# Performance work log

Measured on AMD Instinct MI355X. Metric: run time of the kernel, lower is better.

The kernel has to match this reference:

```python
import jax, jax.numpy as jnp
import numpy as np

N = 1_000_000          # points
C_IN = 10              # decorated point features
C_OUT = 64             # pillar feature channels
S = 30_000             # number of pillars (segments)
EPS = 1e-3             # BatchNorm1d eps


def setup_inputs() -> dict:
    key = jax.random.key(0)
    ks = jax.random.split(key, 8)
    inputs = jax.random.normal(ks[0], (N, C_IN), dtype=jnp.float32)
    # every pillar gets ~N/S points; sorted, all segments non-empty
    unq_inv = jnp.sort(jnp.arange(N, dtype=jnp.int32) % S)
    W_lin = jax.random.normal(ks[1], (C_OUT, C_IN), dtype=jnp.float32) * 0.3
    gamma = 1.0 + 0.1 * jax.random.normal(ks[2], (C_OUT,), dtype=jnp.float32)
    beta = 0.1 * jax.random.normal(ks[3], (C_OUT,), dtype=jnp.float32)
    dw1 = jax.random.normal(ks[4], (C_OUT,), dtype=jnp.float32) * 0.5      # depthwise 1x1 conv (groups=C)
    pw1 = jax.random.normal(ks[5], (C_OUT, C_OUT), dtype=jnp.float32) * 0.1  # pointwise 1x1 conv
    dw2 = jax.random.normal(ks[6], (C_OUT,), dtype=jnp.float32) * 0.5
    pw2 = jax.random.normal(ks[7], (C_OUT, C_OUT), dtype=jnp.float32) * 0.1
    return {"inputs": inputs, "unq_inv": unq_inv, "W_lin": W_lin,
            "gamma": gamma, "beta": beta, "dw1": dw1, "pw1": pw1,
            "dw2": dw2, "pw2": pw2}


def reference(inputs, unq_inv, W_lin, gamma, beta, dw1, pw1, dw2, pw2):
    # Linear (no bias) -> BN (training-mode batch stats) -> ReLU
    x = inputs @ W_lin.T                                   # [N, C]
    mu = jnp.mean(x, axis=0)
    var = jnp.mean(jnp.square(x - mu), axis=0)             # biased var, as torch BN
    x = (x - mu) * jax.lax.rsqrt(var + EPS) * gamma + beta
    x = jax.nn.relu(x)

    # MAFF attention: local branch (depthwise scale -> swish -> 1x1 conv)
    s = x * dw1                                            # groups=C 1x1 conv == per-channel scale
    xl = (s * jax.nn.sigmoid(s)) @ pw1.T                   # [N, C]
    # global branch: avg-pool over points -> depthwise scale -> relu -> 1x1 conv
    g = jnp.mean(x, axis=0)                                # [C]
    xg = pw2 @ jax.nn.relu(dw2 * g)                        # [C]
    wei = jax.nn.sigmoid(xl + xg)                          # broadcast [N,C] + [C]
    xi = x * (1.0 + wei)

    # segment reductions keyed by pillar id (scatter_max + scatter_sum)
    x_max = jax.ops.segment_max(xi, unq_inv, num_segments=S,
                                indices_are_sorted=True)
    x_sum = jax.ops.segment_sum(xi, unq_inv, num_segments=S,
                                indices_are_sorted=True)
    return x_max + x_sum                                   # [S, C]
```

## Files before the change

kernel.cpp:

```cpp
#include <hip/hip_runtime.h>
#include <math.h>

#define N_PTS   1000000
#define CI      10
#define C       64
#define NSEG    30000
#define BN_EPS  1e-3f


using f32x4 = __attribute__((ext_vector_type(4))) float;
using s16x8 = __attribute__((ext_vector_type(8))) short;

__device__ inline short f2bf(float x) {
    unsigned u = __float_as_uint(x);
    unsigned r = (u + 0x7fffu + ((u >> 16) & 1u)) >> 16;
    return (short)r;
}
__device__ inline unsigned pack_trunc(float lo, float hi) {
    return (__float_as_uint(hi) & 0xffff0000u) | (__float_as_uint(lo) >> 16);
}
__device__ inline float frcp(float x) { return __builtin_amdgcn_rcpf(x); }

__global__ void __launch_bounds__(256) k_moments(const float* __restrict__ inp,
                                                 const int* __restrict__ idx,
                                                 float* __restrict__ ws,
                                                 int* __restrict__ starts) {
    const int tid = threadIdx.x;
    float v[65];
#pragma unroll
    for (int k = 0; k < 65; ++k) v[k] = 0.f;

    for (int p = blockIdx.x * blockDim.x + tid; p < N_PTS; p += gridDim.x * blockDim.x) {
        const float2* r2 = (const float2*)(inp + (size_t)p * CI);
        float2 a0 = r2[0], a1 = r2[1], a2 = r2[2], a3 = r2[3], a4 = r2[4];
        float r[CI] = {a0.x, a0.y, a1.x, a1.y, a2.x, a2.y, a3.x, a3.y, a4.x, a4.y};
#pragma unroll
        for (int i = 0; i < CI; ++i) v[i] += r[i];
        int kk = 10;
#pragma unroll
        for (int i = 0; i < CI; ++i)
#pragma unroll
            for (int j = i; j < CI; ++j) { v[kk] = fmaf(r[i], r[j], v[kk]); ++kk; }

        int iv = idx[p];
        if (p == 0) starts[0] = 0;
        else if (idx[p - 1] != iv) starts[iv] = p;
    }

#pragma unroll
    for (int k = 0; k < 65; ++k) {
#pragma unroll
        for (int off = 32; off >= 1; off >>= 1)
            v[k] += __shfl_xor(v[k], off, 64);
    }
    __shared__ float red[4 * 65];
    const int wv = tid >> 6, ln = tid & 63;
    if (ln == 0) {
#pragma unroll
        for (int k = 0; k < 65; ++k) red[wv * 65 + k] = v[k];
    }
    __syncthreads();
    if (tid < 65)
        atomicAdd(&ws[tid], red[tid] + red[65 + tid] + red[130 + tid] + red[195 + tid]);
}

__global__ void k_finalize(const float* __restrict__ W,
                           const float* __restrict__ gamma,
                           const float* __restrict__ beta,
                           float* __restrict__ ws) {
    const int c = threadIdx.x;
    float w[CI];
#pragma unroll
    for (int i = 0; i < CI; ++i) w[i] = W[c * CI + i];
    const float inv_n = 1.f / (float)N_PTS;

    float mu = 0.f;
#pragma unroll
    for (int i = 0; i < CI; ++i) mu = fmaf(w[i], ws[i], mu);
    mu *= inv_n;

    float ex2 = 0.f;
    int kk = 10;
#pragma unroll
    for (int i = 0; i < CI; ++i)
#pragma unroll
        for (int j = i; j < CI; ++j) {
            float m = ws[kk];
            float t = w[i] * w[j] * m;
            ex2 += (i == j) ? t : 2.f * t;
            ++kk;
        }
    ex2 *= inv_n;

    float var = ex2 - mu * mu;
    float rstd = rsqrtf(var + BN_EPS);
    float a = rstd * gamma[c];
    ws[128 + c] = a;
    ws[192 + c] = beta[c] - mu * a;
#pragma unroll
    for (int i = 0; i < CI; ++i) ws[384 + c * CI + i] = a * w[i];
}

__global__ void __launch_bounds__(256) k_gstats(const float* __restrict__ inp,
                                                float* __restrict__ ws) {
    const int tid  = threadIdx.x;
    const int oct  = tid & 7;
    const int slot = (tid & 63) >> 3;

    float w[8][CI], bv[8];
#pragma unroll
    for (int j = 0; j < 8; ++j) {
        const int c = oct * 8 + j;
#pragma unroll
        for (int i = 0; i < CI; ++i) w[j][i] = ws[384 + c * CI + i];
        bv[j] = ws[192 + c];
    }

    float acc[8];
#pragma unroll
    for (int j = 0; j < 8; ++j) acc[j] = 0.f;

    const int wid = (blockIdx.x * blockDim.x + tid) >> 6;
    const int nw  = (gridDim.x * blockDim.x) >> 6;
    for (int pb = wid * 8; pb < N_PTS; pb += nw * 8) {
        const int p = pb + slot;
        const float2* r2 = (const float2*)(inp + (size_t)p * CI);
        float2 a0 = r2[0], a1 = r2[1], a2 = r2[2], a3 = r2[3], a4 = r2[4];
        float r[CI] = {a0.x, a0.y, a1.x, a1.y, a2.x, a2.y, a3.x, a3.y, a4.x, a4.y};
#pragma unroll
        for (int j = 0; j < 8; ++j) {
            float x = bv[j];
#pragma unroll
            for (int i = 0; i < CI; ++i) x = fmaf(w[j][i], r[i], x);
            acc[j] += fmaxf(x, 0.f);
        }
    }

#pragma unroll
    for (int j = 0; j < 8; ++j) {
        acc[j] += __shfl_xor(acc[j], 8, 64);
        acc[j] += __shfl_xor(acc[j], 16, 64);
        acc[j] += __shfl_xor(acc[j], 32, 64);
    }
    __shared__ float red[4 * 64];
    const int wv = tid >> 6, ln = tid & 63;
    if (ln < 8) {
#pragma unroll
        for (int j = 0; j < 8; ++j) red[wv * 64 + ln * 8 + j] = acc[j];
    }
    __syncthreads();
    if (tid < 64)
        atomicAdd(&ws[256 + tid], red[tid] + red[64 + tid] + red[128 + tid] + red[192 + tid]);
}

__global__ void k_xg(const float* __restrict__ dw2,
                     const float* __restrict__ pw2,
                     float* __restrict__ ws) {
    __shared__ float t[C];
    const int c = threadIdx.x;
    float g = ws[256 + c] * (1.f / (float)N_PTS);
    t[c] = fmaxf(dw2[c] * g, 0.f);
    __syncthreads();
    float acc = 0.f;
#pragma unroll
    for (int k = 0; k < C; ++k) acc = fmaf(pw2[c * C + k], t[k], acc);
    ws[320 + c] = acc;
}

#define LD 68
__global__ void __launch_bounds__(128) k_main(const float* __restrict__ inp,
                                              const float* __restrict__ dw1,
                                              const float* __restrict__ pw1,
                                              const float* __restrict__ ws,
                                              const int* __restrict__ starts,
                                              float* __restrict__ out) {
    const int tid  = threadIdx.x;
    const int wv   = tid >> 6;
    const int lane = tid & 63;
    const int m = lane & 15;
    const int q = lane >> 4;

    s16x8 wfr[4];
#pragma unroll
    for (int nt = 0; nt < 4; ++nt) {
        s16x8 t;
#pragma unroll
        for (int j = 0; j < 8; ++j) {
            int k = 8 * q + j;
            t[j] = (k < CI) ? f2bf(ws[384 + (nt * 16 + m) * CI + k]) : (short)0;
        }
        wfr[nt] = t;
    }

    s16x8 bfr[4][2];
#pragma unroll
    for (int nt = 0; nt < 4; ++nt)
#pragma unroll
        for (int kc = 0; kc < 2; ++kc) {
            const float* src = pw1 + (nt * 16 + m) * C + kc * 32 + q * 8;
            float4 p0 = *(const float4*)src;
            float4 p1 = *(const float4*)(src + 4);
            s16x8 t;
            t[0] = f2bf(p0.x); t[1] = f2bf(p0.y); t[2] = f2bf(p0.z); t[3] = f2bf(p0.w);
            t[4] = f2bf(p1.x); t[5] = f2bf(p1.y); t[6] = f2bf(p1.z); t[7] = f2bf(p1.w);
            bfr[nt][kc] = t;
        }

    float bb[4], d1v[4], xgv[4];
#pragma unroll
    for (int nt = 0; nt < 4; ++nt) {
        bb[nt]  = ws[192 + nt * 16 + m];
        d1v[nt] = dw1[nt * 16 + m];
        xgv[nt] = ws[320 + nt * 16 + m];
    }

    __shared__ float sb[2][16 * LD];
    float* my = sb[wv];
    const f32x4 zero = {0.f, 0.f, 0.f, 0.f};

    const int gw = blockIdx.x * 2 + wv;
    for (int s = gw; s < NSEG; s += 15000) {
        const int start = starts[s];
        const int end   = (s + 1 < NSEG) ? starts[s + 1] : N_PTS;

        float sm[4]  = {0.f, 0.f, 0.f, 0.f};
        float mxv[4] = {-INFINITY, -INFINITY, -INFINITY, -INFINITY};

        for (int base = start; base < end; base += 16) {
            const int nb = min(16, end - base);

            const int p = min(base + m, N_PTS - 1);
            const float* row = inp + (size_t)p * CI;
            s16x8 afr = {0, 0, 0, 0, 0, 0, 0, 0};
            if (q == 0) {
                float2 r0 = *(const float2*)(row + 0);
                float2 r1 = *(const float2*)(row + 2);
                float2 r2 = *(const float2*)(row + 4);
                float2 r3 = *(const float2*)(row + 6);
                afr[0] = f2bf(r0.x); afr[1] = f2bf(r0.y);
                afr[2] = f2bf(r1.x); afr[3] = f2bf(r1.y);
                afr[4] = f2bf(r2.x); afr[5] = f2bf(r2.y);
                afr[6] = f2bf(r3.x); afr[7] = f2bf(r3.y);
            } else if (q == 1) {
                float2 r4 = *(const float2*)(row + 8);
                afr[0] = f2bf(r4.x); afr[1] = f2bf(r4.y);
            }

            f32x4 xt[4];
#pragma unroll
            for (int nt = 0; nt < 4; ++nt)
                xt[nt] = __builtin_amdgcn_mfma_f32_16x16x32_bf16(afr, wfr[nt], zero, 0, 0, 0);

            float xn[4][4];
#pragma unroll
            for (int nt = 0; nt < 4; ++nt)
#pragma unroll
                for (int r = 0; r < 4; ++r) {
                    float x = fmaxf(xt[nt][r] + bb[nt], 0.f);
                    xn[nt][r] = x;
                    float sg = x * d1v[nt];
                    float sw = sg * frcp(1.f + __expf(-sg));
                    my[(4 * q + r) * LD + nt * 16 + m] = sw;
                }
            __threadfence_block();

            s16x8 av[2];
#pragma unroll
            for (int kc = 0; kc < 2; ++kc) {
                const float* src = &my[m * LD + kc * 32 + q * 8];
                float4 p0 = *(const float4*)src;
                float4 p1 = *(const float4*)(src + 4);
                union { s16x8 v; unsigned u[4]; } t;
                t.u[0] = pack_trunc(p0.x, p0.y);
                t.u[1] = pack_trunc(p0.z, p0.w);
                t.u[2] = pack_trunc(p1.x, p1.y);
                t.u[3] = pack_trunc(p1.z, p1.w);
                av[kc] = t.v;
            }

            f32x4 xl[4];
#pragma unroll
            for (int nt = 0; nt < 4; ++nt) {
                xl[nt] = __builtin_amdgcn_mfma_f32_16x16x32_bf16(av[0], bfr[nt][0], zero, 0, 0, 0);
                xl[nt] = __builtin_amdgcn_mfma_f32_16x16x32_bf16(av[1], bfr[nt][1], xl[nt], 0, 0, 0);
            }
            __threadfence_block();

#pragma unroll
            for (int nt = 0; nt < 4; ++nt)
#pragma unroll
                for (int r = 0; r < 4; ++r) {
                    float v   = xl[nt][r] + xgv[nt];
                    float wei = frcp(1.f + __expf(-v));
                    float x   = xn[nt][r];
                    float xi  = fmaf(x, wei, x);
                    bool act  = (4 * q + r) < nb;
                    sm[nt]  += act ? xi : 0.f;
                    mxv[nt]  = fmaxf(mxv[nt], act ? xi : -INFINITY);
                }
        }

#pragma unroll
        for (int nt = 0; nt < 4; ++nt) {
            sm[nt] += __shfl_xor(sm[nt], 16, 64);
            sm[nt] += __shfl_xor(sm[nt], 32, 64);
            mxv[nt] = fmaxf(mxv[nt], __shfl_xor(mxv[nt], 16, 64));
            mxv[nt] = fmaxf(mxv[nt], __shfl_xor(mxv[nt], 32, 64));
        }
        float S = sm[0], M = mxv[0];
        if (q == 1) { S = sm[1]; M = mxv[1]; }
        if (q == 2) { S = sm[2]; M = mxv[2]; }
        if (q == 3) { S = sm[3]; M = mxv[3]; }
        out[(size_t)s * C + lane] = S + M;
    }
}

extern "C" void kernel_launch(void* const* d_in, const int* in_sizes, int n_in,
                              void* d_out, int out_size, void* d_ws, size_t ws_size,
                              hipStream_t stream) {
    const float* inp   = (const float*)d_in[0];
    const int*   unq   = (const int*)d_in[1];
    const float* W     = (const float*)d_in[2];
    const float* gamma = (const float*)d_in[3];
    const float* beta  = (const float*)d_in[4];
    const float* dw1   = (const float*)d_in[5];
    const float* pw1   = (const float*)d_in[6];
    const float* dw2   = (const float*)d_in[7];
    const float* pw2   = (const float*)d_in[8];
    float* out = (float*)d_out;
    float* ws  = (float*)d_ws;
    int* starts = (int*)ws + 1024;

    hipMemsetAsync(ws, 0, 384 * sizeof(float), stream);

    k_moments <<<512, 256, 0, stream>>>(inp, unq, ws, starts);
    k_finalize<<<1,   64,  0, stream>>>(W, gamma, beta, ws);
    k_gstats  <<<256, 256, 0, stream>>>(inp, ws);
    k_xg      <<<1,   64,  0, stream>>>(dw2, pw2, ws);
    k_main    <<<7500, 128, 0, stream>>>(inp, dw1, pw1, ws, starts, out);
}
```

Before: 310.2 us.

## Pack multiple pillars per wave and use MFMA for global-stat pass

k_main now gives each wave six consecutive segments and walks their points as one contiguous stream of 16-row tiles, splitting a tile across a segment boundary with masks and flushing per segment. This fills MFMA tiles that per-segment processing left partly empty and adds software prefetch of the next tile's rows. k_gstats is rewritten to compute the linear layer with bf16 MFMA and a prefetched row load, replacing the scalar FMA loop, and grid sizes are adjusted. The cost is more complex boundary logic and extra bf16 rounding in the global mean.

```diff
diff --git a/kernel.cpp b/kernel.cpp
--- a/kernel.cpp
+++ b/kernel.cpp
@@ -104,50 +104,81 @@
 __global__ void __launch_bounds__(256) k_gstats(const float* __restrict__ inp,
                                                 float* __restrict__ ws) {
     const int tid  = threadIdx.x;
-    const int oct  = tid & 7;
-    const int slot = (tid & 63) >> 3;
-
-    float w[8][CI], bv[8];
-#pragma unroll
-    for (int j = 0; j < 8; ++j) {
-        const int c = oct * 8 + j;
-#pragma unroll
-        for (int i = 0; i < CI; ++i) w[j][i] = ws[384 + c * CI + i];
-        bv[j] = ws[192 + c];
-    }
-
-    float acc[8];
-#pragma unroll
-    for (int j = 0; j < 8; ++j) acc[j] = 0.f;
-
-    const int wid = (blockIdx.x * blockDim.x + tid) >> 6;
-    const int nw  = (gridDim.x * blockDim.x) >> 6;
-    for (int pb = wid * 8; pb < N_PTS; pb += nw * 8) {
-        const int p = pb + slot;
-        const float2* r2 = (const float2*)(inp + (size_t)p * CI);
-        float2 a0 = r2[0], a1 = r2[1], a2 = r2[2], a3 = r2[3], a4 = r2[4];
-        float r[CI] = {a0.x, a0.y, a1.x, a1.y, a2.x, a2.y, a3.x, a3.y, a4.x, a4.y};
+    const int wv   = tid >> 6;
+    const int lane = tid & 63;
+    const int m = lane & 15;
+    const int q = lane >> 4;
+
+    s16x8 wfr[4];
+#pragma unroll
+    for (int nt = 0; nt < 4; ++nt) {
+        s16x8 t;
 #pragma unroll
         for (int j = 0; j < 8; ++j) {
-            float x = bv[j];
-#pragma unroll
-            for (int i = 0; i < CI; ++i) x = fmaf(w[j][i], r[i], x);
-            acc[j] += fmaxf(x, 0.f);
-        }
-    }
-
-#pragma unroll
-    for (int j = 0; j < 8; ++j) {
-        acc[j] += __shfl_xor(acc[j], 8, 64);
-        acc[j] += __shfl_xor(acc[j], 16, 64);
-        acc[j] += __shfl_xor(acc[j], 32, 64);
-    }
+            int k = 8 * q + j;
+            t[j] = (k < CI) ? f2bf(ws[384 + (nt * 16 + m) * CI + k]) : (short)0;
+        }
+        wfr[nt] = t;
+    }
+    float bb[4];
+#pragma unroll
+    for (int nt = 0; nt < 4; ++nt) bb[nt] = ws[192 + nt * 16 + m];
+
+    const int wid = blockIdx.x * 4 + wv;
+    const int nw  = gridDim.x * 4;
+    const int NB  = N_PTS / 16;
+
+    float2 P0, P1, P2, P3;
+    auto loadrows = [&](int pb) {
+        const float* row = inp + (size_t)(pb + m) * CI;
+        if (q == 0) {
+            P0 = *(const float2*)(row);     P1 = *(const float2*)(row + 2);
+            P2 = *(const float2*)(row + 4); P3 = *(const float2*)(row + 6);
+        } else if (q == 1) {
+            P0 = *(const float2*)(row + 8);
+        }
+    };
+    P0 = P1 = P2 = P3 = make_float2(0.f, 0.f);
+
+    float sm[4] = {0.f, 0.f, 0.f, 0.f};
+    const f32x4 zero = {0.f, 0.f, 0.f, 0.f};
+
+    if (wid < NB) loadrows(wid * 16);
+    for (int b = wid; b < NB; b += nw) {
+        float2 L0 = P0, L1 = P1, L2 = P2, L3 = P3;
+        if (b + nw < NB) loadrows((b + nw) * 16);
+
+        union { s16x8 v; unsigned u[4]; } t;
+        t.v = s16x8{0, 0, 0, 0, 0, 0, 0, 0};
+        if (q < 2) t.u[0] = pack_trunc(L0.x, L0.y);
+        if (q == 0) {
+            t.u[1] = pack_trunc(L1.x, L1.y);
+            t.u[2] = pack_trunc(L2.x, L2.y);
+            t.u[3] = pack_trunc(L3.x, L3.y);
+        }
+
+        f32x4 xt[4];
+#pragma unroll
+        for (int nt = 0; nt < 4; ++nt) {
+            xt[nt] = __builtin_amdgcn_mfma_f32_16x16x32_bf16(t.v, wfr[nt], zero, 0, 0, 0);
+#pragma unroll
+            for (int r = 0; r < 4; ++r)
+                sm[nt] += fmaxf(xt[nt][r] + bb[nt], 0.f);
+        }
+    }
+
+#pragma unroll
+    for (int nt = 0; nt < 4; ++nt) {
+        sm[nt] += __shfl_xor(sm[nt], 16, 64);
+        sm[nt] += __shfl_xor(sm[nt], 32, 64);
+    }
+    float S = sm[0];
+    if (q == 1) S = sm[1];
+    if (q == 2) S = sm[2];
+    if (q == 3) S = sm[3];
+
     __shared__ float red[4 * 64];
-    const int wv = tid >> 6, ln = tid & 63;
-    if (ln < 8) {
-#pragma unroll
-        for (int j = 0; j < 8; ++j) red[wv * 64 + ln * 8 + j] = acc[j];
-    }
+    red[wv * 64 + lane] = S;
     __syncthreads();
     if (tid < 64)
         atomicAdd(&ws[256 + tid], red[tid] + red[64 + tid] + red[128 + tid] + red[192 + tid]);
@@ -168,6 +199,7 @@
 }
 
 #define LD 68
+#define SEGW 6
 __global__ void __launch_bounds__(128) k_main(const float* __restrict__ inp,
                                               const float* __restrict__ dw1,
                                               const float* __restrict__ pw1,
@@ -191,7 +223,6 @@
         }
         wfr[nt] = t;
     }
-
     s16x8 bfr[4][2];
 #pragma unroll
     for (int nt = 0; nt < 4; ++nt)
@@ -218,88 +249,25 @@
     float* my = sb[wv];
     const f32x4 zero = {0.f, 0.f, 0.f, 0.f};
 
-    const int gw = blockIdx.x * 2 + wv;
-    for (int s = gw; s < NSEG; s += 15000) {
-        const int start = starts[s];
-        const int end   = (s + 1 < NSEG) ? starts[s + 1] : N_PTS;
-
-        float sm[4]  = {0.f, 0.f, 0.f, 0.f};
-        float mxv[4] = {-INFINITY, -INFINITY, -INFINITY, -INFINITY};
-
-        for (int base = start; base < end; base += 16) {
-            const int nb = min(16, end - base);
-
-            const int p = min(base + m, N_PTS - 1);
-            const float* row = inp + (size_t)p * CI;
-            s16x8 afr = {0, 0, 0, 0, 0, 0, 0, 0};
-            if (q == 0) {
-                float2 r0 = *(const float2*)(row + 0);
-                float2 r1 = *(const float2*)(row + 2);
-                float2 r2 = *(const float2*)(row + 4);
-                float2 r3 = *(const float2*)(row + 6);
-                afr[0] = f2bf(r0.x); afr[1] = f2bf(r0.y);
-                afr[2] = f2bf(r1.x); afr[3] = f2bf(r1.y);
-                afr[4] = f2bf(r2.x); afr[5] = f2bf(r2.y);
-                afr[6] = f2bf(r3.x); afr[7] = f2bf(r3.y);
-            } else if (q == 1) {
-                float2 r4 = *(const float2*)(row + 8);
-                afr[0] = f2bf(r4.x); afr[1] = f2bf(r4.y);
-            }
-
-            f32x4 xt[4];
-#pragma unroll
-            for (int nt = 0; nt < 4; ++nt)
-                xt[nt] = __builtin_amdgcn_mfma_f32_16x16x32_bf16(afr, wfr[nt], zero, 0, 0, 0);
-
-            float xn[4][4];
-#pragma unroll
-            for (int nt = 0; nt < 4; ++nt)
-#pragma unroll
-                for (int r = 0; r < 4; ++r) {
-                    float x = fmaxf(xt[nt][r] + bb[nt], 0.f);
-                    xn[nt][r] = x;
-                    float sg = x * d1v[nt];
-                    float sw = sg * frcp(1.f + __expf(-sg));
-                    my[(4 * q + r) * LD + nt * 16 + m] = sw;
-                }
-            __threadfence_block();
-
-            s16x8 av[2];
-#pragma unroll
-            for (int kc = 0; kc < 2; ++kc) {
-                const float* src = &my[m * LD + kc * 32 + q * 8];
-                float4 p0 = *(const float4*)src;
-                float4 p1 = *(const float4*)(src + 4);
-                union { s16x8 v; unsigned u[4]; } t;
-                t.u[0] = pack_trunc(p0.x, p0.y);
-                t.u[1] = pack_trunc(p0.z, p0.w);
-                t.u[2] = pack_trunc(p1.x, p1.y);
-                t.u[3] = pack_trunc(p1.z, p1.w);
-                av[kc] = t.v;
-            }
-
-            f32x4 xl[4];
-#pragma unroll
-            for (int nt = 0; nt < 4; ++nt) {
-                xl[nt] = __builtin_amdgcn_mfma_f32_16x16x32_bf16(av[0], bfr[nt][0], zero, 0, 0, 0);
-                xl[nt] = __builtin_amdgcn_mfma_f32_16x16x32_bf16(av[1], bfr[nt][1], xl[nt], 0, 0, 0);
-            }
-            __threadfence_block();
-
-#pragma unroll
-            for (int nt = 0; nt < 4; ++nt)
-#pragma unroll
-                for (int r = 0; r < 4; ++r) {
-                    float v   = xl[nt][r] + xgv[nt];
-                    float wei = frcp(1.f + __expf(-v));
-                    float x   = xn[nt][r];
-                    float xi  = fmaf(x, wei, x);
-                    bool act  = (4 * q + r) < nb;
-                    sm[nt]  += act ? xi : 0.f;
-                    mxv[nt]  = fmaxf(mxv[nt], act ? xi : -INFINITY);
-                }
-        }
-
+    const int w  = blockIdx.x * 2 + wv;
+    const int s0 = w * SEGW;
+
+    int st[SEGW + 1];
+#pragma unroll
+    for (int i = 0; i <= SEGW; ++i) {
+        int s = s0 + i;
+        st[i] = (s >= NSEG) ? N_PTS : starts[s];
+    }
+    const int start   = st[0];
+    const int end_all = st[SEGW];
+
+    int cur = s0, nsel = 1;
+    int end_cur = st[1];
+
+    float sm[4]  = {0.f, 0.f, 0.f, 0.f};
+    float mxv[4] = {-INFINITY, -INFINITY, -INFINITY, -INFINITY};
+
+    auto flushseg = [&](int s) {
 #pragma unroll
         for (int nt = 0; nt < 4; ++nt) {
             sm[nt] += __shfl_xor(sm[nt], 16, 64);
@@ -312,6 +280,141 @@
         if (q == 2) { S = sm[2]; M = mxv[2]; }
         if (q == 3) { S = sm[3]; M = mxv[3]; }
         out[(size_t)s * C + lane] = S + M;
+#pragma unroll
+        for (int nt = 0; nt < 4; ++nt) { sm[nt] = 0.f; mxv[nt] = -INFINITY; }
+    };
+    auto advance_end = [&]() {
+        ++nsel;
+        int e = st[1];
+        if (nsel >= 2) e = st[2];
+        if (nsel >= 3) e = st[3];
+        if (nsel >= 4) e = st[4];
+        if (nsel >= 5) e = st[5];
+        if (nsel >= 6) e = st[6];
+        end_cur = e;
+    };
+
+    float2 P0, P1, P2, P3;
+    auto loadrows = [&](int pb) {
+        const float* row = inp + (size_t)min(pb + m, N_PTS - 1) * CI;
+        if (q == 0) {
+            P0 = *(const float2*)(row);     P1 = *(const float2*)(row + 2);
+            P2 = *(const float2*)(row + 4); P3 = *(const float2*)(row + 6);
+        } else if (q == 1) {
+            P0 = *(const float2*)(row + 8);
+        }
+    };
+    P0 = P1 = P2 = P3 = make_float2(0.f, 0.f);
+    loadrows(start);
+
+    for (int base = start; base < end_all; base += 16) {
+        float2 L0 = P0, L1 = P1, L2 = P2, L3 = P3;
+        if (base + 16 < end_all) loadrows(base + 16);
+
+        const int nb = min(16, end_all - base);
+
+        union { s16x8 v; unsigned u[4]; } t;
+        t.v = s16x8{0, 0, 0, 0, 0, 0, 0, 0};
+        if (q < 2) t.u[0] = pack_trunc(L0.x, L0.y);
+        if (q == 0) {
+            t.u[1] = pack_trunc(L1.x, L1.y);
+            t.u[2] = pack_trunc(L2.x, L2.y);
+            t.u[3] = pack_trunc(L3.x, L3.y);
+        }
+
+        f32x4 xt[4];
+#pragma unroll
+        for (int nt = 0; nt < 4; ++nt)
+            xt[nt] = __builtin_amdgcn_mfma_f32_16x16x32_bf16(t.v, wfr[nt], zero, 0, 0, 0);
+
+        float xn[4][4];
+#pragma unroll
+        for (int nt = 0; nt < 4; ++nt)
+#pragma unroll
+            for (int r = 0; r < 4; ++r) {
+                float x = fmaxf(xt[nt][r] + bb[nt], 0.f);
+                xn[nt][r] = x;
+                float sg = x * d1v[nt];
+                float sw = sg * frcp(1.f + __expf(-sg));
+                my[(4 * q + r) * LD + nt * 16 + m] = sw;
+            }
+        __threadfence_block();
+
+        s16x8 av[2];
+#pragma unroll
+        for (int kc = 0; kc < 2; ++kc) {
+            const float* src = &my[m * LD + kc * 32 + q * 8];
+            float4 p0 = *(const float4*)src;
+            float4 p1 = *(const float4*)(src + 4);
+            union { s16x8 v; unsigned u[4]; } tt;
+            tt.u[0] = pack_trunc(p0.x, p0.y);
+            tt.u[1] = pack_trunc(p0.z, p0.w);
+            tt.u[2] = pack_trunc(p1.x, p1.y);
+            tt.u[3] = pack_trunc(p1.z, p1.w);
+            av[kc] = tt.v;
+        }
+
+        f32x4 xi[4];
+#pragma unroll
+        for (int nt = 0; nt < 4; ++nt) {
+            xi[nt] = __builtin_amdgcn_mfma_f32_16x16x32_bf16(av[0], bfr[nt][0], zero, 0, 0, 0);
+            xi[nt] = __builtin_amdgcn_mfma_f32_16x16x32_bf16(av[1], bfr[nt][1], xi[nt], 0, 0, 0);
+        }
+        __threadfence_block();
+
+#pragma unroll
+        for (int nt = 0; nt < 4; ++nt)
+#pragma unroll
+            for (int r = 0; r < 4; ++r) {
+                float v   = xi[nt][r] + xgv[nt];
+                float wei = frcp(1.f + __expf(-v));
+                float x   = xn[nt][r];
+                xi[nt][r] = fmaf(x, wei, x);
+            }
+
+        const int fin = base + nb;
+        if (fin <= end_cur) {
+            if (nb == 16) {
+#pragma unroll
+                for (int nt = 0; nt < 4; ++nt)
+#pragma unroll
+                    for (int r = 0; r < 4; ++r) {
+                        sm[nt] += xi[nt][r];
+                        mxv[nt] = fmaxf(mxv[nt], xi[nt][r]);
+                    }
+            } else {
+#pragma unroll
+                for (int nt = 0; nt < 4; ++nt)
+#pragma unroll
+                    for (int r = 0; r < 4; ++r) {
+                        bool act = (4 * q + r) < nb;
+                        sm[nt] += act ? xi[nt][r] : 0.f;
+                        mxv[nt] = fmaxf(mxv[nt], act ? xi[nt][r] : -INFINITY);
+                    }
+            }
+            if (fin == end_cur) { flushseg(cur); ++cur; advance_end(); }
+        } else {
+            const int B = end_cur - base;
+#pragma unroll
+            for (int nt = 0; nt < 4; ++nt)
+#pragma unroll
+                for (int r = 0; r < 4; ++r) {
+                    bool act = (4 * q + r) < B;
+                    sm[nt] += act ? xi[nt][r] : 0.f;
+                    mxv[nt] = fmaxf(mxv[nt], act ? xi[nt][r] : -INFINITY);
+                }
+            flushseg(cur); ++cur;
+#pragma unroll
+            for (int nt = 0; nt < 4; ++nt)
+#pragma unroll
+                for (int r = 0; r < 4; ++r) {
+                    int pt = 4 * q + r;
+                    bool act = (pt >= B) && (pt < nb);
+                    sm[nt] += act ? xi[nt][r] : 0.f;
+                    mxv[nt] = fmaxf(mxv[nt], act ? xi[nt][r] : -INFINITY);
+                }
+            advance_end();
+        }
     }
 }
 
@@ -333,9 +436,9 @@
 
     hipMemsetAsync(ws, 0, 384 * sizeof(float), stream);
 
-    k_moments <<<512, 256, 0, stream>>>(inp, unq, ws, starts);
-    k_finalize<<<1,   64,  0, stream>>>(W, gamma, beta, ws);
-    k_gstats  <<<256, 256, 0, stream>>>(inp, ws);
-    k_xg      <<<1,   64,  0, stream>>>(dw2, pw2, ws);
-    k_main    <<<7500, 128, 0, stream>>>(inp, dw1, pw1, ws, starts, out);
-}
+    k_moments <<<1024, 256, 0, stream>>>(inp, unq, ws, starts);
+    k_finalize<<<1,    64,  0, stream>>>(W, gamma, beta, ws);
+    k_gstats  <<<512,  256, 0, stream>>>(inp, ws);
+    k_xg      <<<1,    64,  0, stream>>>(dw2, pw2, ws);
+    k_main    <<<2500, 128, 0, stream>>>(inp, dw1, pw1, ws, starts, out);
+}
```

Measured after the change: 302.3 us. 2.6% less time.
